# Optimization experiments

Measured on AMD Instinct MI355X. Metric: run time of the kernel, lower is better.

Reference implementation:

```python
import jax, jax.numpy as jnp
import numpy as np

B, S, HID = 2, 2048, 2048
NH, NKV, D = 32, 4, 64
N_REP = NH // NKV
EPS = 1e-6
ROPE_THETA = 10000.0


def _rotate_half(x):
    h = x.shape[-1] // 2
    return jnp.concatenate([-x[..., h:], x[..., :h]], axis=-1)


def _rmsnorm(x, gamma):
    # RMSNorm over last dim (head_dim)
    return x * jax.lax.rsqrt(jnp.mean(x * x, axis=-1, keepdims=True) + EPS) * gamma


def setup_inputs() -> dict:
    key = jax.random.key(0)
    ks = jax.random.split(key, 8)
    hidden_states = jax.random.normal(ks[0], (B, S, HID), dtype=jnp.float32)
    # rotary cos/sin tables, shape [B, S, D]
    pos = jnp.arange(S, dtype=jnp.float32)
    inv_freq = 1.0 / (ROPE_THETA ** (jnp.arange(0, D, 2, dtype=jnp.float32) / D))
    freqs = pos[:, None] * inv_freq[None, :]            # [S, D/2]
    emb = jnp.concatenate([freqs, freqs], axis=-1)      # [S, D]
    cos = jnp.broadcast_to(jnp.cos(emb)[None], (B, S, D))
    sin = jnp.broadcast_to(jnp.sin(emb)[None], (B, S, D))
    sc = 0.02
    Wq = jax.random.normal(ks[1], (NH * D, HID), dtype=jnp.float32) * sc
    Wk = jax.random.normal(ks[2], (NKV * D, HID), dtype=jnp.float32) * sc
    Wv = jax.random.normal(ks[3], (NKV * D, HID), dtype=jnp.float32) * sc
    Wg = jax.random.normal(ks[4], (NH * D, HID), dtype=jnp.float32) * sc
    Wo = jax.random.normal(ks[5], (HID, NH * D), dtype=jnp.float32) * sc
    q_gamma = jnp.ones((D,), dtype=jnp.float32)
    k_gamma = jnp.ones((D,), dtype=jnp.float32)
    return dict(hidden_states=hidden_states, cos=cos, sin=sin,
                Wq=Wq, Wk=Wk, Wv=Wv, Wg=Wg, Wo=Wo,
                q_gamma=q_gamma, k_gamma=k_gamma)


def reference(hidden_states, cos, sin, Wq, Wk, Wv, Wg, Wo, q_gamma, k_gamma):
    b, s, _ = hidden_states.shape
    q = (hidden_states @ Wq.T).reshape(b, s, NH, D)
    k = (hidden_states @ Wk.T).reshape(b, s, NKV, D)
    v = (hidden_states @ Wv.T).reshape(b, s, NKV, D)
    gate = hidden_states @ Wg.T                       # [B, S, NH*D]
    # per-head RMSNorm on q/k
    q = _rmsnorm(q, q_gamma)
    k = _rmsnorm(k, k_gamma)
    # [B, H, S, D]
    q = q.transpose(0, 2, 1, 3)
    k = k.transpose(0, 2, 1, 3)
    v = v.transpose(0, 2, 1, 3)
    # RoPE (unsqueeze_dim=1)
    c = cos[:, None, :, :]
    sn = sin[:, None, :, :]
    q = q * c + _rotate_half(q) * sn
    k = k * c + _rotate_half(k) * sn
    # GQA: repeat kv heads
    kr = jnp.repeat(k, N_REP, axis=1)
    vr = jnp.repeat(v, N_REP, axis=1)
    scaling = D ** -0.5
    scores = jnp.einsum('bhqd,bhkd->bhqk', q, kr) * scaling
    w = jax.nn.softmax(scores.astype(jnp.float32), axis=-1).astype(q.dtype)
    out = jnp.einsum('bhqk,bhkd->bhqd', w, vr)
    out = out.transpose(0, 2, 1, 3).reshape(b, s, NH * D)
    out = out * jax.nn.sigmoid(gate)
    return out @ Wo.T
```

## Files before the change

### kernel.cpp

```cpp
#include <hip/hip_runtime.h>


#define LOG2E 1.44269504088896340736f

typedef __attribute__((ext_vector_type(4))) float f32x4;
typedef __attribute__((ext_vector_type(8))) short bf16x8;

__device__ __forceinline__ float bf2f(unsigned short u) {
  union { unsigned u; float f; } x; x.u = ((unsigned)u) << 16; return x.f;
}
__device__ __forceinline__ unsigned short f2bf(float f) {
  union { float f; unsigned u; } x; x.f = f;
  unsigned r = x.u + 0x7fffu + ((x.u >> 16) & 1u);
  return (unsigned short)(r >> 16);
}

__device__ __forceinline__ void async16(void* lds, const void* g) {
  __builtin_amdgcn_global_load_lds(
      (const __attribute__((address_space(1))) unsigned*)g,
      (__attribute__((address_space(3))) unsigned*)lds, 16, 0, 0);
}
__device__ __forceinline__ void lds_fence() {
  __asm__ volatile("s_waitcnt lgkmcnt(0)" ::: "memory");
}

__global__ __launch_bounds__(256) void cvt_all(
    const float* __restrict__ s0, const float* __restrict__ s1,
    const float* __restrict__ s2, const float* __restrict__ s3,
    const float* __restrict__ s4, const float* __restrict__ s5,
    unsigned short* __restrict__ d0, unsigned short* __restrict__ d1,
    unsigned short* __restrict__ d2, unsigned short* __restrict__ d3,
    unsigned short* __restrict__ d4, unsigned short* __restrict__ d5) {
  long i = (long)blockIdx.x * 256 + threadIdx.x;
  const float* s; unsigned short* d; long off;
  if      (i < 2097152) { s = s0; d = d0; off = 0; }
  else if (i < 3145728) { s = s1; d = d1; off = 2097152; }
  else if (i < 3276800) { s = s2; d = d2; off = 3145728; }
  else if (i < 3407872) { s = s3; d = d3; off = 3276800; }
  else if (i < 4456448) { s = s4; d = d4; off = 3407872; }
  else                  { s = s5; d = d5; off = 4456448; }
  long j = i - off;
  float4 v = reinterpret_cast<const float4*>(s)[j];
  ushort4 u;
  u.x = f2bf(v.x); u.y = f2bf(v.y); u.z = f2bf(v.z); u.w = f2bf(v.w);
  reinterpret_cast<ushort4*>(d)[j] = u;
}

__device__ __forceinline__ void gemm_main_big(
    const unsigned short* __restrict__ A, const unsigned short* __restrict__ W,
    int m0, int n0, unsigned short* lds, f32x4 acc[4][4]) {
  const int tid = threadIdx.x;
  const int w = tid >> 6, l = tid & 63, quad = l >> 4, l16 = l & 15;
  const int l7 = l16 & 7;
  const int wm = (w & 1) * 64, wn = (w >> 1) * 64;
  const int rlo = tid >> 3, ch = tid & 7;

  const f32x4 Z4 = {0.f, 0.f, 0.f, 0.f};
#pragma unroll
  for (int i = 0; i < 4; i++)
#pragma unroll
    for (int j = 0; j < 4; j++) acc[i][j] = Z4;

  const unsigned short* gA = A + (size_t)(m0 + rlo) * 2048 + ((ch ^ (rlo & 7)) * 8);
  const unsigned short* gB = W + (size_t)(n0 + rlo) * 2048 + ((ch ^ (rlo & 7)) * 8);

  int arow[4], brow[4];
#pragma unroll
  for (int mt = 0; mt < 4; mt++) arow[mt] = (wm + mt * 16 + l16) * 64;
#pragma unroll
  for (int nt = 0; nt < 4; nt++) brow[nt] = (wn + nt * 16 + l16) * 64;
  const int x0 = (quad ^ l7) * 8;
  const int x1 = ((4 + quad) ^ l7) * 8;

  unsigned short* const bA = lds;
  unsigned short* const bB = lds + 16384;

  async16(bA + tid * 8,          gA);
  async16(bA + 4096 + tid * 8,   gA + 131072);
  async16(bB + tid * 8,          gB);
  async16(bB + 4096 + tid * 8,   gB + 131072);
  async16(bB + 8192 + tid * 8,   gB + 262144);
  async16(bB + 12288 + tid * 8,  gB + 393216);
  async16(bB + 16384 + tid * 8,  gB + 64);
  async16(bB + 20480 + tid * 8,  gB + 131072 + 64);
  async16(bB + 24576 + tid * 8,  gB + 262144 + 64);
  async16(bB + 28672 + tid * 8,  gB + 393216 + 64);
  __asm__ volatile("s_waitcnt vmcnt(4)" ::: "memory");
  __builtin_amdgcn_s_barrier();

  int cb = 0;
  for (int t = 0; t < 32; ++t) {
    unsigned short* cbA = bA + (t & 1) * 8192;
    unsigned short* cbB = bB + cb * 16384;

    if (t < 31) {
      unsigned short* nA = bA + ((t + 1) & 1) * 8192;
      const int ko = (t + 1) * 64;
      async16(nA + tid * 8,        gA + ko);
      async16(nA + 4096 + tid * 8, gA + 131072 + ko);
    }
    bf16x8 a0[4], b0[4];
#pragma unroll
    for (int mt = 0; mt < 4; mt++)
      a0[mt] = *(const bf16x8*)&cbA[arow[mt] + x0];
#pragma unroll
    for (int nt = 0; nt < 4; nt++)
      b0[nt] = *(const bf16x8*)&cbB[brow[nt] + x0];
    __builtin_amdgcn_s_barrier();
    __asm__ volatile("s_waitcnt lgkmcnt(0)" ::: "memory");
    __builtin_amdgcn_sched_barrier(0);
    __builtin_amdgcn_s_setprio(1);
#pragma unroll
    for (int mt = 0; mt < 4; mt++)
#pragma unroll
      for (int nt = 0; nt < 4; nt++)
        acc[mt][nt] = __builtin_amdgcn_mfma_f32_16x16x32_bf16(
            a0[mt], b0[nt], acc[mt][nt], 0, 0, 0);
    __builtin_amdgcn_s_setprio(0);
    __builtin_amdgcn_s_barrier();

    if (t < 30) {
      int nb = cb + 2; if (nb >= 3) nb -= 3;
      unsigned short* nB = bB + nb * 16384;
      const int ko = (t + 2) * 64;
      async16(nB + tid * 8,         gB + ko);
      async16(nB + 4096 + tid * 8,  gB + 131072 + ko);
      async16(nB + 8192 + tid * 8,  gB + 262144 + ko);
      async16(nB + 12288 + tid * 8, gB + 393216 + ko);
    }
    bf16x8 a1[4], b1[4];
#pragma unroll
    for (int mt = 0; mt < 4; mt++)
      a1[mt] = *(const bf16x8*)&cbA[arow[mt] + x1];
#pragma unroll
    for (int nt = 0; nt < 4; nt++)
      b1[nt] = *(const bf16x8*)&cbB[brow[nt] + x1];
    __builtin_amdgcn_s_barrier();
    __asm__ volatile("s_waitcnt lgkmcnt(0)" ::: "memory");
    __builtin_amdgcn_sched_barrier(0);
    __builtin_amdgcn_s_setprio(1);
#pragma unroll
    for (int mt = 0; mt < 4; mt++)
#pragma unroll
      for (int nt = 0; nt < 4; nt++)
        acc[mt][nt] = __builtin_amdgcn_mfma_f32_16x16x32_bf16(
            a1[mt], b1[nt], acc[mt][nt], 0, 0, 0);
    __builtin_amdgcn_s_setprio(0);
    if (t < 30) {
      __asm__ volatile("s_waitcnt vmcnt(4)" ::: "memory");
    } else if (t == 30) {
      __asm__ volatile("s_waitcnt vmcnt(0)" ::: "memory");
    }
    __builtin_amdgcn_s_barrier();
    cb++; if (cb == 3) cb = 0;
  }
}

__global__ __launch_bounds__(512, 2) void gemm_qkvg(
    const unsigned short* __restrict__ X,
    const unsigned short* __restrict__ Wq, const unsigned short* __restrict__ Wk,
    const unsigned short* __restrict__ Wv, const unsigned short* __restrict__ Wg,
    const float* __restrict__ cosb, const float* __restrict__ sinb,
    const float* __restrict__ qg, const float* __restrict__ kg,
    unsigned short* __restrict__ Qn, unsigned short* __restrict__ Kn,
    unsigned short* __restrict__ Vt, unsigned short* __restrict__ gate) {
  __shared__ __attribute__((aligned(16))) unsigned short lds[65536];
  const int ny = blockIdx.y;
  const unsigned short* W; int n0, type;
  if (ny < 8)       { W = Wq; n0 = ny * 256;        type = 0; }
  else if (ny == 8) { W = Wk; n0 = 0;               type = 1; }
  else if (ny == 9) { W = Wv; n0 = 0;               type = 2; }
  else              { W = Wg; n0 = (ny - 10) * 256; type = 3; }
  const int m0 = blockIdx.x * 128;

  f32x4 acc[4][4];
  gemm_main_big(X, W, m0, n0, lds, acc);

  const int tid = threadIdx.x;
  const int w = tid >> 6, l = tid & 63, quad = l >> 4, l16 = l & 15;
  const int wm = (w & 1) * 64, wn = (w >> 1) * 64;

  if (type == 3) {
#pragma unroll
    for (int mt = 0; mt < 4; mt++)
#pragma unroll
      for (int r = 0; r < 4; r++) {
        int row = m0 + wm + mt * 16 + quad * 4 + r;
#pragma unroll
        for (int nt = 0; nt < 4; nt++)
          gate[(size_t)row * 2048 + n0 + wn + nt * 16 + l16] =
              f2bf(acc[mt][nt][r]);
      }
    return;
  }
  if (type == 2) {
#pragma unroll
    for (int mt = 0; mt < 4; mt++)
#pragma unroll
      for (int r = 0; r < 4; r++) {
        int row = m0 + wm + mt * 16 + quad * 4 + r;
        int b = row >> 11, s = row & 2047;
#pragma unroll
        for (int nt = 0; nt < 4; nt++) {
          int col = wn + nt * 16 + l16;
          int kvh = col >> 6, d = col & 63;
          Vt[((size_t)(b * 4 + kvh) * 64 + d) * 2048 + s] =
              f2bf(acc[mt][nt][r]);
        }
      }
    return;
  }

  const float* gamma = (type == 0) ? qg : kg;
  const float scale  = (type == 0) ? 0.125f : LOG2E;
  const int hb = (n0 + wn) >> 6;
  float gv[4];
#pragma unroll
  for (int nt = 0; nt < 4; nt++) gv[nt] = gamma[nt * 16 + l16];

#pragma unroll
  for (int mt = 0; mt < 4; mt++)
#pragma unroll
    for (int r = 0; r < 4; r++) {
      int row = m0 + wm + mt * 16 + quad * 4 + r;
      float ss = 0.f;
#pragma unroll
      for (int nt = 0; nt < 4; nt++) {
        float v = acc[mt][nt][r]; ss += v * v;
      }
#pragma unroll
      for (int off = 1; off < 16; off <<= 1) ss += __shfl_xor(ss, off);
      float rr = rsqrtf(ss * (1.0f / 64.0f) + 1e-6f);
      float xn[4];
#pragma unroll
      for (int nt = 0; nt < 4; nt++) xn[nt] = acc[mt][nt][r] * rr * gv[nt];
      int b = row >> 11, s = row & 2047;
      unsigned short* dst = (type == 0)
          ? Qn + ((size_t)(b * 32 + hb) * 2048 + s) * 64
          : Kn + ((size_t)(b * 4 + hb) * 2048 + s) * 64;
#pragma unroll
      for (int nt = 0; nt < 4; nt++) {
        int d = nt * 16 + l16;
        float rot = (nt < 2) ? -xn[nt ^ 2] : xn[nt ^ 2];
        float cv = cosb[(size_t)row * 64 + d];
        float sv = sinb[(size_t)row * 64 + d];
        dst[d] = f2bf((xn[nt] * cv + rot * sv) * scale);
      }
    }
}

__global__ __launch_bounds__(512, 2) void gemm_out_k(
    const unsigned short* __restrict__ A, const unsigned short* __restrict__ W,
    float* __restrict__ C) {
  __shared__ __attribute__((aligned(16))) unsigned short lds[65536];
  const int m0 = blockIdx.x * 128, n0 = blockIdx.y * 256;
  f32x4 acc[4][4];
  gemm_main_big(A, W, m0, n0, lds, acc);
  const int tid = threadIdx.x;
  const int w = tid >> 6, l = tid & 63, quad = l >> 4, l16 = l & 15;
  const int wm = (w & 1) * 64, wn = (w >> 1) * 64;
#pragma unroll
  for (int mt = 0; mt < 4; mt++)
#pragma unroll
    for (int nt = 0; nt < 4; nt++) {
      int row = m0 + wm + mt * 16 + quad * 4;
      int col = n0 + wn + nt * 16 + l16;
#pragma unroll
      for (int r = 0; r < 4; r++)
        C[(size_t)(row + r) * 2048 + col] = acc[mt][nt][r];
    }
}

__global__ __launch_bounds__(256, 4) void attn(
    const unsigned short* __restrict__ Qn, const unsigned short* __restrict__ Kn,
    const unsigned short* __restrict__ Vt, const unsigned short* __restrict__ gate,
    unsigned short* __restrict__ act) {
  __shared__ __attribute__((aligned(16))) unsigned short smem[20480];
  unsigned short* Ps = smem + 16384;

  const int tid = threadIdx.x, w = tid >> 6, l = tid & 63;
  const int quad = l >> 4, l16 = l & 15, l7 = l16 & 7;
  const int bh = blockIdx.y, b = bh >> 5, h = bh & 31, kvh = h >> 3;
  const int q0 = blockIdx.x * 128;

  const unsigned short* Qg = Qn + ((size_t)(b * 32 + h) * 2048 + q0) * 64;
  const unsigned short* Kg = Kn + (size_t)(b * 4 + kvh) * 2048 * 64;
  const unsigned short* Vg = Vt + (size_t)(b * 4 + kvh) * 64 * 2048;
  unsigned short* Pw = Ps + w * 1024;

  const int kq_src = ((tid & 7) ^ ((tid >> 3) & 7)) * 8;

#pragma unroll
  for (int i = 0; i < 4; i++)
    async16(smem + i * 2048 + tid * 8,
            Qg + (size_t)(i * 32 + (tid >> 3)) * 64 + kq_src);
  __syncthreads();
  bf16x8 qf[2][2];
#pragma unroll
  for (int mt = 0; mt < 2; mt++)
#pragma unroll
    for (int ks = 0; ks < 2; ks++) {
      int row = w * 32 + mt * 16 + l16;
      qf[mt][ks] = *(const bf16x8*)&smem[row * 64 + ((ks * 4 + quad) ^ l7) * 8];
    }
  __syncthreads();

  const f32x4 Z4 = {0.f, 0.f, 0.f, 0.f};
  f32x4 O[2][4];
  float lp[2][4];
#pragma unroll
  for (int mt = 0; mt < 2; mt++) {
#pragma unroll
    for (int nt = 0; nt < 4; nt++) O[mt][nt] = Z4;
#pragma unroll
    for (int r = 0; r < 4; r++) lp[mt][r] = 0.f;
  }

#pragma unroll
  for (int i = 0; i < 2; i++) {
    async16(smem + i * 2048 + tid * 8,
            Kg + (size_t)(i * 32 + (tid >> 3)) * 64 + kq_src);
    async16(smem + 4096 + i * 2048 + tid * 8,
            Vg + (size_t)(i * 32 + (tid >> 3)) * 2048 + kq_src);
  }

  for (int kt = 0; kt < 32; kt++) {
    __syncthreads();

    if (kt < 31) {
      unsigned short* nb = smem + ((kt + 1) & 1) * 8192;
      const int s1 = (kt + 1) * 64;
#pragma unroll
      for (int i = 0; i < 2; i++) {
        async16(nb + i * 2048 + tid * 8,
                Kg + (size_t)(s1 + i * 32 + (tid >> 3)) * 64 + kq_src);
        async16(nb + 4096 + i * 2048 + tid * 8,
                Vg + (size_t)(i * 32 + (tid >> 3)) * 2048 + s1 + kq_src);
      }
    }

    unsigned short* Ks  = smem + (kt & 1) * 8192;
    unsigned short* Vts = Ks + 4096;

    f32x4 sc[2][4];
#pragma unroll
    for (int mt = 0; mt < 2; mt++)
#pragma unroll
      for (int nt = 0; nt < 4; nt++) sc[mt][nt] = Z4;
#pragma unroll
    for (int nt = 0; nt < 4; nt++) {
      int row = nt * 16 + l16;
      bf16x8 kf0 = *(const bf16x8*)&Ks[row * 64 + (quad ^ l7) * 8];
      bf16x8 kf1 = *(const bf16x8*)&Ks[row * 64 + ((4 + quad) ^ l7) * 8];
#pragma unroll
      for (int mt = 0; mt < 2; mt++) {
        sc[mt][nt] = __builtin_amdgcn_mfma_f32_16x16x32_bf16(qf[mt][0], kf0, sc[mt][nt], 0, 0, 0);
        sc[mt][nt] = __builtin_amdgcn_mfma_f32_16x16x32_bf16(qf[mt][1], kf1, sc[mt][nt], 0, 0, 0);
      }
    }

#pragma unroll
    for (int ks2 = 0; ks2 < 2; ks2++) {
#pragma unroll
      for (int mt = 0; mt < 2; mt++)
#pragma unroll
        for (int ntl = 0; ntl < 2; ntl++) {
          int nt = ks2 * 2 + ntl;
#pragma unroll
          for (int r = 0; r < 4; r++) {
            float p = __builtin_amdgcn_exp2f(sc[mt][nt][r]);
            union { float f; unsigned u; } x; x.f = p;
            union { unsigned u; float f; } t; t.u = x.u & 0xffff0000u;
            lp[mt][r] += t.f;
            int q = mt * 16 + quad * 4 + r;
            int c = ntl * 2 + (l16 >> 3);
            int phys = c ^ ((q >> 1) & 3);
            Pw[q * 32 + phys * 8 + l7] = (unsigned short)(x.u >> 16);
          }
        }
      lds_fence();

      bf16x8 pf[2];
#pragma unroll
      for (int mt = 0; mt < 2; mt++) {
        int q = mt * 16 + l16;
        int phys = quad ^ ((l16 >> 1) & 3);
        pf[mt] = *(const bf16x8*)&Pw[q * 32 + phys * 8];
      }
#pragma unroll
      for (int nt2 = 0; nt2 < 4; nt2++) {
        int d = nt2 * 16 + l16;
        bf16x8 vf = *(const bf16x8*)&Vts[d * 64 + ((ks2 * 4 + quad) ^ l7) * 8];
#pragma unroll
        for (int mt = 0; mt < 2; mt++)
          O[mt][nt2] = __builtin_amdgcn_mfma_f32_16x16x32_bf16(
              pf[mt], vf, O[mt][nt2], 0, 0, 0);
      }
      lds_fence();
    }
  }

#pragma unroll
  for (int mt = 0; mt < 2; mt++)
#pragma unroll
    for (int r = 0; r < 4; r++) {
      float s = lp[mt][r];
#pragma unroll
      for (int off = 1; off < 16; off <<= 1) s += __shfl_xor(s, off);
      lp[mt][r] = s;
    }

#pragma unroll
  for (int mt = 0; mt < 2; mt++) {
    float inv[4];
#pragma unroll
    for (int r = 0; r < 4; r++) inv[r] = 1.0f / lp[mt][r];
#pragma unroll
    for (int nt = 0; nt < 4; nt++)
#pragma unroll
      for (int r = 0; r < 4; r++) {
        int srow = q0 + w * 32 + mt * 16 + quad * 4 + r;
        int col = h * 64 + nt * 16 + l16;
        size_t off = (size_t)(b * 2048 + srow) * 2048 + col;
        float g = bf2f(gate[off]);
        float sig = 1.0f / (1.0f + __builtin_amdgcn_exp2f(-g * LOG2E));
        act[off] = f2bf(O[mt][nt][r] * inv[r] * sig);
      }
  }
}

extern "C" void kernel_launch(void* const* d_in, const int* in_sizes, int n_in,
                              void* d_out, int out_size, void* d_ws, size_t ws_size,
                              hipStream_t stream) {
  const float* hid  = (const float*)d_in[0];
  const float* cosb = (const float*)d_in[1];
  const float* sinb = (const float*)d_in[2];
  const float* Wq   = (const float*)d_in[3];
  const float* Wk   = (const float*)d_in[4];
  const float* Wv   = (const float*)d_in[5];
  const float* Wg   = (const float*)d_in[6];
  const float* Wo   = (const float*)d_in[7];
  const float* qg   = (const float*)d_in[8];
  const float* kg   = (const float*)d_in[9];
  float* out = (float*)d_out;

  char* ws = (char*)d_ws;
  unsigned short* Xb   = (unsigned short*)(ws);
  unsigned short* WqB  = (unsigned short*)(ws + 16777216);
  unsigned short* WkB  = (unsigned short*)(ws + 25165824);
  unsigned short* WvB  = (unsigned short*)(ws + 26214400);
  unsigned short* WgB  = (unsigned short*)(ws + 27262976);
  unsigned short* WoB  = (unsigned short*)(ws + 35651584);
  unsigned short* gate = (unsigned short*)(ws + 44040192);
  unsigned short* Qn   = (unsigned short*)(ws + 60817408);
  unsigned short* Kn   = (unsigned short*)(ws + 77594624);
  unsigned short* Vt   = (unsigned short*)(ws + 79691776);
  unsigned short* act = WqB;

  cvt_all<<<dim3(21504), dim3(256), 0, stream>>>(
      hid, Wq, Wk, Wv, Wg, Wo, Xb, WqB, WkB, WvB, WgB, WoB);

  gemm_qkvg<<<dim3(32, 18), dim3(512), 0, stream>>>(
      Xb, WqB, WkB, WvB, WgB, cosb, sinb, qg, kg, Qn, Kn, Vt, gate);

  attn<<<dim3(16, 64), dim3(256), 0, stream>>>(Qn, Kn, Vt, gate, act);

  gemm_out_k<<<dim3(32, 8), dim3(512), 0, stream>>>(act, WoB, out);
}
```

Measured before the change: 366.1 us.

## Halve GEMM block threads, double per-warp N tile to 64x128

The two projection GEMMs now run with 256 threads (4 waves) per block instead of 512. Each wave computes a 64x128 output tile, so it holds twice the accumulators and B fragments, and each thread issues twice as many async loads per stage. This raises register reuse of A fragments and lowers the number of waves that share LDS traffic. The cost is lower occupancy (launch bounds 256,1) and much higher register pressure, which risks exposing latency.

```diff
diff --git a/kernel.cpp b/kernel.cpp
--- a/kernel.cpp
+++ b/kernel.cpp
@@ -48,44 +48,43 @@
 
 __device__ __forceinline__ void gemm_main_big(
     const unsigned short* __restrict__ A, const unsigned short* __restrict__ W,
-    int m0, int n0, unsigned short* lds, f32x4 acc[4][4]) {
+    int m0, int n0, unsigned short* lds, f32x4 acc[4][8]) {
   const int tid = threadIdx.x;
   const int w = tid >> 6, l = tid & 63, quad = l >> 4, l16 = l & 15;
   const int l7 = l16 & 7;
-  const int wm = (w & 1) * 64, wn = (w >> 1) * 64;
+  const int wm = (w & 1) * 64, wn = (w >> 1) * 128;
   const int rlo = tid >> 3, ch = tid & 7;
 
   const f32x4 Z4 = {0.f, 0.f, 0.f, 0.f};
 #pragma unroll
   for (int i = 0; i < 4; i++)
 #pragma unroll
-    for (int j = 0; j < 4; j++) acc[i][j] = Z4;
+    for (int j = 0; j < 8; j++) acc[i][j] = Z4;
 
   const unsigned short* gA = A + (size_t)(m0 + rlo) * 2048 + ((ch ^ (rlo & 7)) * 8);
   const unsigned short* gB = W + (size_t)(n0 + rlo) * 2048 + ((ch ^ (rlo & 7)) * 8);
 
-  int arow[4], brow[4];
+  int arow[4], brow[8];
 #pragma unroll
   for (int mt = 0; mt < 4; mt++) arow[mt] = (wm + mt * 16 + l16) * 64;
 #pragma unroll
-  for (int nt = 0; nt < 4; nt++) brow[nt] = (wn + nt * 16 + l16) * 64;
+  for (int nt = 0; nt < 8; nt++) brow[nt] = (wn + nt * 16 + l16) * 64;
   const int x0 = (quad ^ l7) * 8;
   const int x1 = ((4 + quad) ^ l7) * 8;
 
   unsigned short* const bA = lds;
   unsigned short* const bB = lds + 16384;
 
-  async16(bA + tid * 8,          gA);
-  async16(bA + 4096 + tid * 8,   gA + 131072);
-  async16(bB + tid * 8,          gB);
-  async16(bB + 4096 + tid * 8,   gB + 131072);
-  async16(bB + 8192 + tid * 8,   gB + 262144);
-  async16(bB + 12288 + tid * 8,  gB + 393216);
-  async16(bB + 16384 + tid * 8,  gB + 64);
-  async16(bB + 20480 + tid * 8,  gB + 131072 + 64);
-  async16(bB + 24576 + tid * 8,  gB + 262144 + 64);
-  async16(bB + 28672 + tid * 8,  gB + 393216 + 64);
-  __asm__ volatile("s_waitcnt vmcnt(4)" ::: "memory");
+#pragma unroll
+  for (int p = 0; p < 4; p++)
+    async16(bA + p * 2048 + tid * 8, gA + p * 65536);
+#pragma unroll
+  for (int p = 0; p < 8; p++)
+    async16(bB + p * 2048 + tid * 8, gB + p * 65536);
+#pragma unroll
+  for (int p = 0; p < 8; p++)
+    async16(bB + 16384 + p * 2048 + tid * 8, gB + p * 65536 + 64);
+  __asm__ volatile("s_waitcnt vmcnt(8)" ::: "memory");
   __builtin_amdgcn_s_barrier();
 
   int cb = 0;
@@ -96,15 +95,16 @@
     if (t < 31) {
       unsigned short* nA = bA + ((t + 1) & 1) * 8192;
       const int ko = (t + 1) * 64;
-      async16(nA + tid * 8,        gA + ko);
-      async16(nA + 4096 + tid * 8, gA + 131072 + ko);
-    }
-    bf16x8 a0[4], b0[4];
+#pragma unroll
+      for (int p = 0; p < 4; p++)
+        async16(nA + p * 2048 + tid * 8, gA + p * 65536 + ko);
+    }
+    bf16x8 a0[4], b0[8];
 #pragma unroll
     for (int mt = 0; mt < 4; mt++)
       a0[mt] = *(const bf16x8*)&cbA[arow[mt] + x0];
 #pragma unroll
-    for (int nt = 0; nt < 4; nt++)
+    for (int nt = 0; nt < 8; nt++)
       b0[nt] = *(const bf16x8*)&cbB[brow[nt] + x0];
     __builtin_amdgcn_s_barrier();
     __asm__ volatile("s_waitcnt lgkmcnt(0)" ::: "memory");
@@ -113,7 +113,7 @@
 #pragma unroll
     for (int mt = 0; mt < 4; mt++)
 #pragma unroll
-      for (int nt = 0; nt < 4; nt++)
+      for (int nt = 0; nt < 8; nt++)
         acc[mt][nt] = __builtin_amdgcn_mfma_f32_16x16x32_bf16(
             a0[mt], b0[nt], acc[mt][nt], 0, 0, 0);
     __builtin_amdgcn_s_setprio(0);
@@ -123,17 +123,16 @@
       int nb = cb + 2; if (nb >= 3) nb -= 3;
       unsigned short* nB = bB + nb * 16384;
       const int ko = (t + 2) * 64;
-      async16(nB + tid * 8,         gB + ko);
-      async16(nB + 4096 + tid * 8,  gB + 131072 + ko);
-      async16(nB + 8192 + tid * 8,  gB + 262144 + ko);
-      async16(nB + 12288 + tid * 8, gB + 393216 + ko);
-    }
-    bf16x8 a1[4], b1[4];
+#pragma unroll
+      for (int p = 0; p < 8; p++)
+        async16(nB + p * 2048 + tid * 8, gB + p * 65536 + ko);
+    }
+    bf16x8 a1[4], b1[8];
 #pragma unroll
     for (int mt = 0; mt < 4; mt++)
       a1[mt] = *(const bf16x8*)&cbA[arow[mt] + x1];
 #pragma unroll
-    for (int nt = 0; nt < 4; nt++)
+    for (int nt = 0; nt < 8; nt++)
       b1[nt] = *(const bf16x8*)&cbB[brow[nt] + x1];
     __builtin_amdgcn_s_barrier();
     __asm__ volatile("s_waitcnt lgkmcnt(0)" ::: "memory");
@@ -142,12 +141,12 @@
 #pragma unroll
     for (int mt = 0; mt < 4; mt++)
 #pragma unroll
-      for (int nt = 0; nt < 4; nt++)
+      for (int nt = 0; nt < 8; nt++)
         acc[mt][nt] = __builtin_amdgcn_mfma_f32_16x16x32_bf16(
             a1[mt], b1[nt], acc[mt][nt], 0, 0, 0);
     __builtin_amdgcn_s_setprio(0);
     if (t < 30) {
-      __asm__ volatile("s_waitcnt vmcnt(4)" ::: "memory");
+      __asm__ volatile("s_waitcnt vmcnt(8)" ::: "memory");
     } else if (t == 30) {
       __asm__ volatile("s_waitcnt vmcnt(0)" ::: "memory");
     }
@@ -156,7 +155,7 @@
   }
 }
 
-__global__ __launch_bounds__(512, 2) void gemm_qkvg(
+__global__ __launch_bounds__(256, 1) void gemm_qkvg(
     const unsigned short* __restrict__ X,
     const unsigned short* __restrict__ Wq, const unsigned short* __restrict__ Wk,
     const unsigned short* __restrict__ Wv, const unsigned short* __restrict__ Wg,
@@ -173,12 +172,12 @@
   else              { W = Wg; n0 = (ny - 10) * 256; type = 3; }
   const int m0 = blockIdx.x * 128;
 
-  f32x4 acc[4][4];
+  f32x4 acc[4][8];
   gemm_main_big(X, W, m0, n0, lds, acc);
 
   const int tid = threadIdx.x;
   const int w = tid >> 6, l = tid & 63, quad = l >> 4, l16 = l & 15;
-  const int wm = (w & 1) * 64, wn = (w >> 1) * 64;
+  const int wm = (w & 1) * 64, wn = (w >> 1) * 128;
 
   if (type == 3) {
 #pragma unroll
@@ -187,7 +186,7 @@
       for (int r = 0; r < 4; r++) {
         int row = m0 + wm + mt * 16 + quad * 4 + r;
 #pragma unroll
-        for (int nt = 0; nt < 4; nt++)
+        for (int nt = 0; nt < 8; nt++)
           gate[(size_t)row * 2048 + n0 + wn + nt * 16 + l16] =
               f2bf(acc[mt][nt][r]);
       }
@@ -201,7 +200,7 @@
         int row = m0 + wm + mt * 16 + quad * 4 + r;
         int b = row >> 11, s = row & 2047;
 #pragma unroll
-        for (int nt = 0; nt < 4; nt++) {
+        for (int nt = 0; nt < 8; nt++) {
           int col = wn + nt * 16 + l16;
           int kvh = col >> 6, d = col & 63;
           Vt[((size_t)(b * 4 + kvh) * 64 + d) * 2048 + s] =
@@ -213,56 +212,69 @@
 
   const float* gamma = (type == 0) ? qg : kg;
   const float scale  = (type == 0) ? 0.125f : LOG2E;
-  const int hb = (n0 + wn) >> 6;
-  float gv[4];
-#pragma unroll
-  for (int nt = 0; nt < 4; nt++) gv[nt] = gamma[nt * 16 + l16];
+  const int hb0 = (n0 + wn) >> 6;
+  float gv[8];
+#pragma unroll
+  for (int nt = 0; nt < 8; nt++) gv[nt] = gamma[(nt & 3) * 16 + l16];
 
 #pragma unroll
   for (int mt = 0; mt < 4; mt++)
 #pragma unroll
     for (int r = 0; r < 4; r++) {
       int row = m0 + wm + mt * 16 + quad * 4 + r;
-      float ss = 0.f;
+      float ss0 = 0.f, ss1 = 0.f;
 #pragma unroll
       for (int nt = 0; nt < 4; nt++) {
-        float v = acc[mt][nt][r]; ss += v * v;
-      }
-#pragma unroll
-      for (int off = 1; off < 16; off <<= 1) ss += __shfl_xor(ss, off);
-      float rr = rsqrtf(ss * (1.0f / 64.0f) + 1e-6f);
-      float xn[4];
-#pragma unroll
-      for (int nt = 0; nt < 4; nt++) xn[nt] = acc[mt][nt][r] * rr * gv[nt];
+        float v = acc[mt][nt][r]; ss0 += v * v;
+      }
+#pragma unroll
+      for (int nt = 4; nt < 8; nt++) {
+        float v = acc[mt][nt][r]; ss1 += v * v;
+      }
+#pragma unroll
+      for (int off = 1; off < 16; off <<= 1) {
+        ss0 += __shfl_xor(ss0, off);
+        ss1 += __shfl_xor(ss1, off);
+      }
+      float rr0 = rsqrtf(ss0 * (1.0f / 64.0f) + 1e-6f);
+      float rr1 = rsqrtf(ss1 * (1.0f / 64.0f) + 1e-6f);
+      float xn[8];
+#pragma unroll
+      for (int nt = 0; nt < 8; nt++)
+        xn[nt] = acc[mt][nt][r] * ((nt < 4) ? rr0 : rr1) * gv[nt];
       int b = row >> 11, s = row & 2047;
-      unsigned short* dst = (type == 0)
-          ? Qn + ((size_t)(b * 32 + hb) * 2048 + s) * 64
-          : Kn + ((size_t)(b * 4 + hb) * 2048 + s) * 64;
-#pragma unroll
-      for (int nt = 0; nt < 4; nt++) {
-        int d = nt * 16 + l16;
-        float rot = (nt < 2) ? -xn[nt ^ 2] : xn[nt ^ 2];
+      unsigned short* dst0 = (type == 0)
+          ? Qn + ((size_t)(b * 32 + hb0) * 2048 + s) * 64
+          : Kn + ((size_t)(b * 4 + hb0) * 2048 + s) * 64;
+      unsigned short* dst1 = (type == 0)
+          ? Qn + ((size_t)(b * 32 + hb0 + 1) * 2048 + s) * 64
+          : Kn + ((size_t)(b * 4 + hb0 + 1) * 2048 + s) * 64;
+#pragma unroll
+      for (int nt = 0; nt < 8; nt++) {
+        int d = (nt & 3) * 16 + l16;
+        float rot = ((nt & 3) < 2) ? -xn[nt ^ 2] : xn[nt ^ 2];
         float cv = cosb[(size_t)row * 64 + d];
         float sv = sinb[(size_t)row * 64 + d];
-        dst[d] = f2bf((xn[nt] * cv + rot * sv) * scale);
-      }
-    }
-}
-
-__global__ __launch_bounds__(512, 2) void gemm_out_k(
+        float val = (xn[nt] * cv + rot * sv) * scale;
+        ((nt < 4) ? dst0 : dst1)[d] = f2bf(val);
+      }
+    }
+}
+
+__global__ __launch_bounds__(256, 1) void gemm_out_k(
     const unsigned short* __restrict__ A, const unsigned short* __restrict__ W,
     float* __restrict__ C) {
   __shared__ __attribute__((aligned(16))) unsigned short lds[65536];
   const int m0 = blockIdx.x * 128, n0 = blockIdx.y * 256;
-  f32x4 acc[4][4];
+  f32x4 acc[4][8];
   gemm_main_big(A, W, m0, n0, lds, acc);
   const int tid = threadIdx.x;
   const int w = tid >> 6, l = tid & 63, quad = l >> 4, l16 = l & 15;
-  const int wm = (w & 1) * 64, wn = (w >> 1) * 64;
+  const int wm = (w & 1) * 64, wn = (w >> 1) * 128;
 #pragma unroll
   for (int mt = 0; mt < 4; mt++)
 #pragma unroll
-    for (int nt = 0; nt < 4; nt++) {
+    for (int nt = 0; nt < 8; nt++) {
       int row = m0 + wm + mt * 16 + quad * 4;
       int col = n0 + wn + nt * 16 + l16;
 #pragma unroll
@@ -460,10 +472,10 @@
   cvt_all<<<dim3(21504), dim3(256), 0, stream>>>(
       hid, Wq, Wk, Wv, Wg, Wo, Xb, WqB, WkB, WvB, WgB, WoB);
 
-  gemm_qkvg<<<dim3(32, 18), dim3(512), 0, stream>>>(
+  gemm_qkvg<<<dim3(32, 18), dim3(256), 0, stream>>>(
       Xb, WqB, WkB, WvB, WgB, cosb, sinb, qg, kg, Qn, Kn, Vt, gate);
 
   attn<<<dim3(16, 64), dim3(256), 0, stream>>>(Qn, Kn, Vt, gate, act);
 
-  gemm_out_k<<<dim3(32, 8), dim3(512), 0, stream>>>(act, WoB, out);
-}
+  gemm_out_k<<<dim3(32, 8), dim3(256), 0, stream>>>(act, WoB, out);
+}
```

Result: slower. 410.7 us (+12.2%).
